# Kernel tuning notes

Hardware: AMD Instinct MI355X
Metric: run time of the kernel (lower is better)

The kernel has to match this reference:

```python
import jax, jax.numpy as jnp
import numpy as np
import math

GROUPS = 32
EPS = 1e-5

def group_norm(x, w, b):
    B, C, H, W = x.shape
    xg = x.reshape(B, GROUPS, C // GROUPS, H, W)
    mu = xg.mean(axis=(2, 3, 4), keepdims=True)
    var = xg.var(axis=(2, 3, 4), keepdims=True)
    xn = ((xg - mu) * jax.lax.rsqrt(var + EPS)).reshape(B, C, H, W)
    return xn * w[None, :, None, None] + b[None, :, None, None]

def conv1x1(x, w, b):
    # x: [B,Cin,H,W], w: [Cout,Cin], b: [Cout]
    return jnp.einsum('bchw,oc->bohw', x, w) + b[None, :, None, None]

def setup_inputs() -> dict:
    key = jax.random.key(0)
    ks = jax.random.split(key, 8)
    B, C, E, H, W = 8, 256, 512, 64, 64
    x = jax.random.normal(ks[0], (B, C, H, W), dtype=jnp.float32)
    condA = jax.random.normal(ks[1], (B, E, H, W), dtype=jnp.float32)
    gn_x_w = jnp.ones((C,), jnp.float32)
    gn_x_b = jnp.zeros((C,), jnp.float32)
    gn_c_w = jnp.ones((E,), jnp.float32)
    gn_c_b = jnp.zeros((E,), jnp.float32)
    q_w = jax.random.normal(ks[2], (C, C), jnp.float32) * 0.02
    q_b = jnp.zeros((C,), jnp.float32)
    k_w = jax.random.normal(ks[3], (C, E), jnp.float32) * 0.02
    k_b = jnp.zeros((C,), jnp.float32)
    v_w = jax.random.normal(ks[4], (C, E), jnp.float32) * 0.02
    v_b = jnp.zeros((C,), jnp.float32)
    return {"x": x, "condA": condA, "gn_x_w": gn_x_w, "gn_x_b": gn_x_b,
            "gn_c_w": gn_c_w, "gn_c_b": gn_c_b, "q_w": q_w, "q_b": q_b,
            "k_w": k_w, "k_b": k_b, "v_w": v_w, "v_b": v_b}

def reference(x, condA, gn_x_w, gn_x_b, gn_c_w, gn_c_b, q_w, q_b, k_w, k_b, v_w, v_b):
    B, C, H, W = x.shape
    scale = math.sqrt(C)
    h = group_norm(x, gn_x_w, gn_x_b)
    h1 = group_norm(condA, gn_c_w, gn_c_b)
    q = conv1x1(h, q_w, q_b)      # [B,C,H,W]
    k = conv1x1(h1, k_w, k_b)     # [B,C,Hc,Wc]
    v = conv1x1(h1, v_w, v_b)     # [B,C,Hc,Wc]
    qf = q.transpose(0, 2, 3, 1).reshape(B, H * W, C)        # [B,N,C]
    kf = k.reshape(B, C, -1)                                  # [B,C,M]
    vf = v.transpose(0, 2, 3, 1).reshape(B, -1, C)            # [B,M,C]
    attn = jax.nn.softmax(jnp.einsum('bnc,bcm->bnm', qf, kf) / scale, axis=-1)
    out = jnp.einsum('bnm,bmc->bnc', attn, vf)                # [B,N,C]
    return out.reshape(B, H, W, C).transpose(0, 3, 1, 2)
```

## Files before the change

kernel.cpp:

```cpp
#include <hip/hip_runtime.h>


typedef _Float16 half8 __attribute__((ext_vector_type(8)));
typedef _Float16 half4v __attribute__((ext_vector_type(4)));
typedef _Float16 half2v __attribute__((ext_vector_type(2)));
typedef float f32x4 __attribute__((ext_vector_type(4)));
typedef float f32x16 __attribute__((ext_vector_type(16)));
typedef unsigned u32x4v __attribute__((ext_vector_type(4)));

#define MFMA16(a, b, c) __builtin_amdgcn_mfma_f32_16x16x32_f16((a), (b), (c), 0, 0, 0)
#define MFMA32(a, b, c) __builtin_amdgcn_mfma_f32_32x32x16_f16((a), (b), (c), 0, 0, 0)

#define GLOAD_LDS(src, dst)                                                   \
  __builtin_amdgcn_global_load_lds(                                           \
      (const __attribute__((address_space(1))) unsigned*)(src),               \
      (__attribute__((address_space(3))) unsigned*)(dst), 16, 0, 0)

__global__ __launch_bounds__(256) void statswconv_kernel(
    const float* __restrict__ x, const float* __restrict__ condA,
    float* __restrict__ sx, float* __restrict__ sc,
    const float* __restrict__ wq, const float* __restrict__ wk,
    const float* __restrict__ wv, _Float16* __restrict__ wqt,
    _Float16* __restrict__ wkt, _Float16* __restrict__ wvt) {
  int bid = blockIdx.x;
  int t = threadIdx.x;
  if (bid >= 512) {
    int i = (bid - 512) * 256 + t;
    const float* src;
    _Float16* dst;
    int cin, ksbits, gi;
    if (i < 8192) { src = wq; dst = wqt; cin = 256; ksbits = 3; gi = i; }
    else if (i < 24576) { src = wk; dst = wkt; cin = 512; ksbits = 4; gi = i - 8192; }
    else { src = wv; dst = wvt; cin = 512; ksbits = 4; gi = i - 24576; }
    int tile = gi >> 6, g = gi & 63;
    int otile = tile >> ksbits, ks = tile & ((1 << ksbits) - 1);
    int o = otile * 16 + (g & 15), k = ks * 32 + (g >> 4) * 8;
    const float* s = src + (size_t)o * cin + k;
    half8 hv;
#pragma unroll
    for (int j = 0; j < 8; j++) hv[j] = (_Float16)s[j];
    *(half8*)(dst + (size_t)gi * 8) = hv;
    return;
  }
  const float4* src;
  int nf4;
  float* dst;
  float inv_n;
  if (bid < 256) {
    src = (const float4*)(x + (size_t)bid * 32768);
    nf4 = 8192;
    dst = sx + bid * 2;
    inv_n = 1.0f / 32768.0f;
  } else {
    int j = bid - 256;
    src = (const float4*)(condA + (size_t)j * 65536);
    nf4 = 16384;
    dst = sc + j * 2;
    inv_n = 1.0f / 65536.0f;
  }
  float s = 0.f, s2 = 0.f;
  for (int i = t; i < nf4; i += 256) {
    float4 v = src[i];
    s += v.x + v.y + v.z + v.w;
    s2 += v.x * v.x + v.y * v.y + v.z * v.z + v.w * v.w;
  }
#pragma unroll
  for (int m = 1; m <= 32; m <<= 1) {
    s += __shfl_xor(s, m, 64);
    s2 += __shfl_xor(s2, m, 64);
  }
  __shared__ float red[8];
  int w = t >> 6;
  if ((t & 63) == 0) { red[w * 2] = s; red[w * 2 + 1] = s2; }
  __syncthreads();
  if (t == 0) {
    float S = red[0] + red[2] + red[4] + red[6];
    float S2 = red[1] + red[3] + red[5] + red[7];
    float mu = S * inv_n;
    float var = S2 * inv_n - mu * mu;
    dst[0] = mu;
    dst[1] = rsqrtf(var + 1e-5f);
  }
}

__global__ __launch_bounds__(256) void ntrans_kernel(
    const float* __restrict__ x, const float* __restrict__ condA,
    const float* __restrict__ statsx, const float* __restrict__ statsc,
    const float* __restrict__ gxw, const float* __restrict__ gxb,
    const float* __restrict__ gcw, const float* __restrict__ gcb,
    _Float16* __restrict__ hxTt, _Float16* __restrict__ h1Tt) {
  int bid = blockIdx.x;
  const float *src, *stats, *gw, *gb;
  _Float16* dst;
  int CH, gsh, bid2;
  if (bid < 2048) {
    src = x; stats = statsx; gw = gxw; gb = gxb; dst = hxTt;
    CH = 256; gsh = 3; bid2 = bid;
  } else {
    src = condA; stats = statsc; gw = gcw; gb = gcb; dst = h1Tt;
    CH = 512; gsh = 4; bid2 = bid - 2048;
  }
  int b = bid2 & 7, nt = (bid2 >> 3) & 63, ctile = bid2 >> 9;
  int n0 = nt * 64, c0 = ctile * 64;
  int t = threadIdx.x;
  __shared__ float tile[64][65];

  int cl = t >> 2;
  int c = c0 + cl;
  const float* st = stats + ((size_t)b * 32 + (c >> gsh)) * 2;
  float mu = st[0], rs = st[1];
  float a = rs * gw[c];
  float bb = gb[c] - mu * a;
  const float* srow = src + ((size_t)(b * CH + c)) * 4096 + n0 + (t & 3) * 16;
#pragma unroll
  for (int i = 0; i < 4; i++) {
    float4 v = *(const float4*)(srow + 4 * i);
    int nn = (t & 3) * 16 + 4 * i;
    tile[cl][nn + 0] = v.x * a + bb;
    tile[cl][nn + 1] = v.y * a + bb;
    tile[cl][nn + 2] = v.z * a + bb;
    tile[cl][nn + 3] = v.w * a + bb;
  }
  __syncthreads();
  int nl = t >> 2;
  half8 ov[2];
#pragma unroll
  for (int u = 0; u < 2; u++)
#pragma unroll
    for (int i = 0; i < 8; i++) ov[u][i] = (_Float16)tile[(t & 3) * 16 + 8 * u + i][nl];
  int n = n0 + nl;
  size_t tb = ((size_t)b * 256 + (n >> 4)) * (CH >> 5);
  int ca = c0 + (t & 3) * 16;
#pragma unroll
  for (int u = 0; u < 2; u++) {
    int cc = ca + 8 * u;
    size_t addr = ((tb + (cc >> 5)) * 64 + (n & 15) + 16 * ((cc >> 3) & 3)) * 8;
    *(half8*)(dst + addr) = ov[u];
  }
}

__global__ __launch_bounds__(256, 2) void projQ_kernel(
    const _Float16* __restrict__ Ht, const _Float16* __restrict__ Wt,
    const float* __restrict__ bias, _Float16* __restrict__ Qt) {
  int bid = blockIdx.x;
  int b = bid & 7, nt = bid >> 3;
  int t = threadIdx.x, l = t & 63, w = t >> 6;
  int c15 = l & 15, q = l >> 4;

  __shared__ __align__(16) _Float16 hbuf[16384];
  half8* hb = (half8*)hbuf;
  {
    const half8* sg = (const half8*)Ht + (size_t)(b * 256 + nt * 4) * 512;
#pragma unroll
    for (int i = 0; i < 8; i++) hb[t + 256 * i] = sg[t + 256 * i];
  }
  __syncthreads();

  const half8* wt8 = (const half8*)Wt;
#pragma unroll
  for (int p = 0; p < 2; p++) {
    int oa = (p * 4 + w) * 2;
    f32x4 acc[2][4] = {};
#pragma unroll
    for (int ks = 0; ks < 8; ks++) {
      half8 af0 = wt8[((size_t)(oa + 0) * 8 + ks) * 64 + l];
      half8 af1 = wt8[((size_t)(oa + 1) * 8 + ks) * 64 + l];
#pragma unroll
      for (int nt2 = 0; nt2 < 4; nt2++) {
        half8 bf = hb[(nt2 * 8 + ks) * 64 + l];
        acc[0][nt2] = MFMA16(af0, bf, acc[0][nt2]);
        acc[1][nt2] = MFMA16(af1, bf, acc[1][nt2]);
      }
    }
#pragma unroll
    for (int j = 0; j < 2; j++) {
      int o4 = (oa + j) * 16 + 4 * q;
      f32x4 bv = *(const f32x4*)(bias + o4);
#pragma unroll
      for (int nt2 = 0; nt2 < 4; nt2++) {
        half4v hv;
#pragma unroll
        for (int r = 0; r < 4; r++) hv[r] = (_Float16)((acc[j][nt2][r] + bv[r]) * 0.0625f);
        size_t addr = ((((size_t)b * 128 + nt * 2 + (nt2 >> 1)) * 16 + (oa + j)) * 64 +
                       (nt2 & 1) * 16 + c15 + 32 * (q >> 1)) * 8 + (q & 1) * 4;
        *(half4v*)(Qt + addr) = hv;
      }
    }
  }
}

__global__ __launch_bounds__(256, 2) void projKV_kernel(
    const _Float16* __restrict__ Ht, const _Float16* __restrict__ Wk,
    const _Float16* __restrict__ Wv, const float* __restrict__ kb,
    const float* __restrict__ vb, _Float16* __restrict__ Kt,
    _Float16* __restrict__ Vt) {
  int bid = blockIdx.x;
  int b = bid & 7, mt = bid >> 3;
  int m0 = mt * 64;
  int t = threadIdx.x, l = t & 63, w = t >> 6;
  int c15 = l & 15, q = l >> 4;

  __shared__ __align__(16) _Float16 hbuf[32768];
  half8* hb = (half8*)hbuf;
  {
    const half8* sg = (const half8*)Ht + (size_t)(b * 256 + mt * 4) * 1024;
#pragma unroll
    for (int i = 0; i < 16; i++) hb[t + 256 * i] = sg[t + 256 * i];
  }
  __syncthreads();

  const half8* wk8 = (const half8*)Wk;
  const half8* wv8 = (const half8*)Wv;
#pragma unroll
  for (int p = 0; p < 2; p++) {
    int oa = (p * 4 + w) * 2;
    f32x4 acck[2][4] = {};
    f32x4 accv[4][2] = {};
#pragma unroll
    for (int ks = 0; ks < 16; ks++) {
      half8 kf0 = wk8[((size_t)(oa + 0) * 16 + ks) * 64 + l];
      half8 kf1 = wk8[((size_t)(oa + 1) * 16 + ks) * 64 + l];
      half8 vf0 = wv8[((size_t)(oa + 0) * 16 + ks) * 64 + l];
      half8 vf1 = wv8[((size_t)(oa + 1) * 16 + ks) * 64 + l];
#pragma unroll
      for (int nt2 = 0; nt2 < 4; nt2++) {
        half8 lf = hb[(nt2 * 16 + ks) * 64 + l];
        acck[0][nt2] = MFMA16(kf0, lf, acck[0][nt2]);
        acck[1][nt2] = MFMA16(kf1, lf, acck[1][nt2]);
        accv[nt2][0] = MFMA16(lf, vf0, accv[nt2][0]);
        accv[nt2][1] = MFMA16(lf, vf1, accv[nt2][1]);
      }
    }
#pragma unroll
    for (int j = 0; j < 2; j++) {
      int o4 = (oa + j) * 16 + 4 * q;
      f32x4 bv = *(const f32x4*)(kb + o4);
#pragma unroll
      for (int nt2 = 0; nt2 < 4; nt2++) {
        half4v hv;
#pragma unroll
        for (int r = 0; r < 4; r++) hv[r] = (_Float16)(acck[j][nt2][r] + bv[r]);
        size_t addr = ((((size_t)b * 128 + mt * 2 + (nt2 >> 1)) * 16 + (oa + j)) * 64 +
                       (nt2 & 1) * 16 + c15 + 32 * (q >> 1)) * 8 + (q & 1) * 4;
        *(half4v*)(Kt + addr) = hv;
      }
    }
#pragma unroll
    for (int nt2 = 0; nt2 < 4; nt2++) {
      int m = m0 + nt2 * 16 + 4 * q;
      size_t mbase = ((size_t)b * 256 + (m >> 4)) * 8;
#pragma unroll
      for (int j = 0; j < 2; j++) {
        int c = (oa + j) * 16 + c15;
        float bs = vb[c];
        half4v hv;
#pragma unroll
        for (int r = 0; r < 4; r++) hv[r] = (_Float16)(accv[nt2][j][r] + bs);
        size_t addr = ((mbase + (c >> 5)) * 64 + (c & 31) + ((q >> 1) << 5)) * 8 + (q & 1) * 4;
        *(half4v*)(Vt + addr) = hv;
      }
    }
  }
}

__global__ __launch_bounds__(256, 2) void attn_kernel(
    const _Float16* __restrict__ Qt, const _Float16* __restrict__ Kt,
    const _Float16* __restrict__ Vt, float* __restrict__ out,
    float* __restrict__ O1, float* __restrict__ l0g,
    float* __restrict__ l1g) {
  int bid = blockIdx.x;
  int b = bid & 7, nt = (bid >> 3) & 31, ms = bid >> 8;
  int n0 = nt * 128;
  int t = threadIdx.x, l = t & 63, nh = t >> 6;
  int l31 = l & 31, h = l >> 5;
  int it0 = ms * 64, it1 = it0 + 64;

  __shared__ __align__(16) _Float16 kbuf[2][8192];
  __shared__ __align__(16) _Float16 vbuf[2][8192];

  half8 qf[16];
  {
    const half8* qt8 =
        (const half8*)Qt + ((size_t)(b * 128 + nt * 4 + nh) * 16) * 64 + l;
#pragma unroll
    for (int ks = 0; ks < 16; ks++) qf[ks] = qt8[ks * 64];
  }

  const _Float16* ksrc = Kt + (size_t)b * 1048576;
  const _Float16* vsrc = Vt + (size_t)b * 1048576;

  f32x16 acc[8] = {};
  float l_part = 0.f;

#define STAGE(it)                                                          \
  {                                                                        \
    int bs_ = (it) & 1;                                                    \
    const _Float16* ks_ = ksrc + (size_t)(it) * 8192;                      \
    const _Float16* vs_ = vsrc + (size_t)(it) * 8192;                      \
    _Float16* kd_ = &kbuf[bs_][0];                                         \
    _Float16* vd_ = &vbuf[bs_][0];                                         \
    _Pragma("unroll") for (int r_ = 0; r_ < 4; r_++) {                     \
      GLOAD_LDS(ks_ + (t + 256 * r_) * 8, kd_ + (t + 256 * r_) * 8);       \
      GLOAD_LDS(vs_ + (t + 256 * r_) * 8, vd_ + (t + 256 * r_) * 8);       \
    }                                                                      \
  }

  STAGE(it0);
  __syncthreads();

  for (int it = it0; it < it1; it++) {
    int cur = it & 1;
    if (it + 1 < it1) STAGE(it + 1);

    const half8* kb = (const half8*)&kbuf[cur][0] + l;
    const half8* vb8 = (const half8*)&vbuf[cur][0] + l;

    f32x16 s = {};
#pragma unroll
    for (int g = 0; g < 4; g++) {
      half8 kf[4];
#pragma unroll
      for (int i = 0; i < 4; i++) kf[i] = kb[(g * 4 + i) * 64];
      __builtin_amdgcn_s_setprio(1);
#pragma unroll
      for (int i = 0; i < 4; i++) s = MFMA32(kf[i], qf[g * 4 + i], s);
      __builtin_amdgcn_s_setprio(0);
    }

    unsigned uo[8];
#pragma unroll
    for (int k2 = 0; k2 < 8; k2++) {
      float e0 = __expf(s[2 * k2]);
      float e1 = __expf(s[2 * k2 + 1]);
      l_part += e0 + e1;
      half2v h2 = {(_Float16)e0, (_Float16)e1};
      uo[k2] = __builtin_bit_cast(unsigned, h2);
    }
    unsigned x0 = uo[0], y0 = uo[2];
    asm("v_permlane32_swap_b32 %0, %1" : "+v"(x0), "+v"(y0));
    unsigned x1 = uo[1], y1 = uo[3];
    asm("v_permlane32_swap_b32 %0, %1" : "+v"(x1), "+v"(y1));
    unsigned x2 = uo[4], y2 = uo[6];
    asm("v_permlane32_swap_b32 %0, %1" : "+v"(x2), "+v"(y2));
    unsigned x3 = uo[5], y3 = uo[7];
    asm("v_permlane32_swap_b32 %0, %1" : "+v"(x3), "+v"(y3));
    u32x4v P0 = {x0, x1, y0, y1};
    u32x4v P1 = {x2, x3, y2, y3};
    half8 pf0 = __builtin_bit_cast(half8, P0);
    half8 pf1 = __builtin_bit_cast(half8, P1);

#pragma unroll
    for (int u = 0; u < 2; u++) {
      const half8* vv = vb8 + u * 512;
      half8 pfu = u ? pf1 : pf0;
#pragma unroll
      for (int g = 0; g < 2; g++) {
        half8 vf[4];
#pragma unroll
        for (int i = 0; i < 4; i++) vf[i] = vv[(g * 4 + i) * 64];
        __builtin_amdgcn_s_setprio(1);
#pragma unroll
        for (int i = 0; i < 4; i++)
          acc[g * 4 + i] = MFMA32(pfu, vf[i], acc[g * 4 + i]);
        __builtin_amdgcn_s_setprio(0);
      }
    }
    __syncthreads();
  }
#undef STAGE

  {
    float v = l_part + __shfl_xor(l_part, 32, 64);
    float* lG = ms ? l1g : l0g;
    if (l < 32) lG[b * 4096 + n0 + nh * 32 + l] = v;
  }
  float* ob = ms ? O1 : out;
#pragma unroll
  for (int cb = 0; cb < 8; cb++) {
    int c = cb * 32 + l31;
    float* orow = ob + ((size_t)(b * 256 + c)) * 4096 + n0 + nh * 32 + 4 * h;
#pragma unroll
    for (int k2 = 0; k2 < 4; k2++) {
      f32x4 o4;
#pragma unroll
      for (int r = 0; r < 4; r++) o4[r] = acc[cb][4 * k2 + r];
      *(f32x4*)(orow + 8 * k2) = o4;
    }
  }
}

__global__ __launch_bounds__(256) void combine_kernel(
    float* __restrict__ out, const float* __restrict__ O1,
    const float* __restrict__ l0g, const float* __restrict__ l1g) {
  size_t i = (size_t)blockIdx.x * 256 + threadIdx.x;
  f32x4 a = ((const f32x4*)out)[i];
  f32x4 b4 = ((const f32x4*)O1)[i];
  int bidx = (int)(i >> 18);
  int n4 = (int)(i & 1023);
  f32x4 La = ((const f32x4*)l0g)[bidx * 1024 + n4];
  f32x4 Lb = ((const f32x4*)l1g)[bidx * 1024 + n4];
  f32x4 r;
#pragma unroll
  for (int j = 0; j < 4; j++) r[j] = (a[j] + b4[j]) / (La[j] + Lb[j]);
  ((f32x4*)out)[i] = r;
}

extern "C" void kernel_launch(void* const* d_in, const int* in_sizes, int n_in,
                              void* d_out, int out_size, void* d_ws,
                              size_t ws_size, hipStream_t stream) {
  const float* x = (const float*)d_in[0];
  const float* condA = (const float*)d_in[1];
  const float* gxw = (const float*)d_in[2];
  const float* gxb = (const float*)d_in[3];
  const float* gcw = (const float*)d_in[4];
  const float* gcb = (const float*)d_in[5];
  const float* qw = (const float*)d_in[6];
  const float* qb = (const float*)d_in[7];
  const float* kw = (const float*)d_in[8];
  const float* kb = (const float*)d_in[9];
  const float* vw = (const float*)d_in[10];
  const float* vb = (const float*)d_in[11];
  float* out = (float*)d_out;

  char* ws = (char*)d_ws;
  float* statsx = (float*)(ws);
  float* statsc = (float*)(ws + 2048);
  _Float16* wqt = (_Float16*)(ws + 4096);
  _Float16* wkt = (_Float16*)(ws + 135168);
  _Float16* wvt = (_Float16*)(ws + 397312);
  char* p = ws + 659456;
  _Float16* hxTt = (_Float16*)p; p += (size_t)8 * 4096 * 256 * 2;
  _Float16* h1Tt = (_Float16*)p; p += (size_t)8 * 4096 * 512 * 2;
  _Float16* Qt = (_Float16*)p;   p += (size_t)8 * 4096 * 256 * 2;
  _Float16* Kt = (_Float16*)p;   p += (size_t)8 * 4096 * 256 * 2;
  _Float16* Vt = (_Float16*)p;

  float* O1 = (float*)(ws + 659456);
  float* l0g = (float*)(ws + 659456 + (size_t)33554432);
  float* l1g = (float*)(ws + 659456 + (size_t)33554432 + 131072);

  statswconv_kernel<<<672, 256, 0, stream>>>(x, condA, statsx, statsc,
                                             qw, kw, vw, wqt, wkt, wvt);
  ntrans_kernel<<<6144, 256, 0, stream>>>(x, condA, statsx, statsc,
                                          gxw, gxb, gcw, gcb, hxTt, h1Tt);
  projQ_kernel<<<512, 256, 0, stream>>>(hxTt, wqt, qb, Qt);
  projKV_kernel<<<512, 256, 0, stream>>>(h1Tt, wkt, wvt, kb, vb, Kt, Vt);
  attn_kernel<<<512, 256, 0, stream>>>(Qt, Kt, Vt, out, O1, l0g, l1g);
  combine_kernel<<<8192, 256, 0, stream>>>(out, O1, l0g, l1g);
}
```

Baseline: 383.2 us.

## Load V fragments directly from global into registers instead of LDS staging

The attention kernel stops staging V tiles through double-buffered shared memory. Each wave now reads its V MFMA operands straight from global memory into registers, issuing half before the QK^T step so the latency overlaps with compute. This halves LDS usage and removes the LDS write/read traffic for V. In exchange, every wave (4 per block) fetches the same V data redundantly from global/L2, register pressure rises with 16 extra half8 values, and the load latency may be exposed.

```diff
diff --git a/kernel.cpp b/kernel.cpp
--- a/kernel.cpp
+++ b/kernel.cpp
@@ -276,7 +276,6 @@
   int it0 = ms * 64, it1 = it0 + 64;
 
   __shared__ __align__(16) _Float16 kbuf[2][8192];
-  __shared__ __align__(16) _Float16 vbuf[2][8192];
 
   half8 qf[16];
   {
@@ -287,33 +286,34 @@
   }
 
   const _Float16* ksrc = Kt + (size_t)b * 1048576;
-  const _Float16* vsrc = Vt + (size_t)b * 1048576;
+  const half8* vg = (const half8*)(Vt + (size_t)b * 1048576) + l;
 
   f32x16 acc[8] = {};
   float l_part = 0.f;
 
-#define STAGE(it)                                                          \
+#define STAGE_K(it)                                                        \
   {                                                                        \
     int bs_ = (it) & 1;                                                    \
     const _Float16* ks_ = ksrc + (size_t)(it) * 8192;                      \
-    const _Float16* vs_ = vsrc + (size_t)(it) * 8192;                      \
     _Float16* kd_ = &kbuf[bs_][0];                                         \
-    _Float16* vd_ = &vbuf[bs_][0];                                         \
     _Pragma("unroll") for (int r_ = 0; r_ < 4; r_++) {                     \
       GLOAD_LDS(ks_ + (t + 256 * r_) * 8, kd_ + (t + 256 * r_) * 8);       \
-      GLOAD_LDS(vs_ + (t + 256 * r_) * 8, vd_ + (t + 256 * r_) * 8);       \
     }                                                                      \
   }
 
-  STAGE(it0);
+  STAGE_K(it0);
   __syncthreads();
 
   for (int it = it0; it < it1; it++) {
     int cur = it & 1;
-    if (it + 1 < it1) STAGE(it + 1);
+    if (it + 1 < it1) STAGE_K(it + 1);
 
     const half8* kb = (const half8*)&kbuf[cur][0] + l;
-    const half8* vb8 = (const half8*)&vbuf[cur][0] + l;
+    const half8* vt = vg + (size_t)it * 1024;
+
+    half8 vfA[8];
+#pragma unroll
+    for (int i = 0; i < 8; i++) vfA[i] = vt[i * 64];
 
     f32x16 s = {};
 #pragma unroll
@@ -349,25 +349,20 @@
     half8 pf0 = __builtin_bit_cast(half8, P0);
     half8 pf1 = __builtin_bit_cast(half8, P1);
 
-#pragma unroll
-    for (int u = 0; u < 2; u++) {
-      const half8* vv = vb8 + u * 512;
-      half8 pfu = u ? pf1 : pf0;
-#pragma unroll
-      for (int g = 0; g < 2; g++) {
-        half8 vf[4];
-#pragma unroll
-        for (int i = 0; i < 4; i++) vf[i] = vv[(g * 4 + i) * 64];
-        __builtin_amdgcn_s_setprio(1);
-#pragma unroll
-        for (int i = 0; i < 4; i++)
-          acc[g * 4 + i] = MFMA32(pfu, vf[i], acc[g * 4 + i]);
-        __builtin_amdgcn_s_setprio(0);
-      }
-    }
+    half8 vfB[8];
+#pragma unroll
+    for (int i = 0; i < 8; i++) vfB[i] = vt[(8 + i) * 64];
+    __builtin_amdgcn_s_setprio(1);
+#pragma unroll
+    for (int cb = 0; cb < 8; cb++) acc[cb] = MFMA32(pf0, vfA[cb], acc[cb]);
+    __builtin_amdgcn_s_setprio(0);
+    __builtin_amdgcn_s_setprio(1);
+#pragma unroll
+    for (int cb = 0; cb < 8; cb++) acc[cb] = MFMA32(pf1, vfB[cb], acc[cb]);
+    __builtin_amdgcn_s_setprio(0);
     __syncthreads();
   }
-#undef STAGE
+#undef STAGE_K
 
   {
     float v = l_part + __shfl_xor(l_part, 32, 64);
```

Result: slower. 459.3 us (+19.9%).

## Fuse group-norm apply and transpose into Q/KV projection kernels

Applied to the files above, without the earlier changes.

Removes the separate normalize-and-transpose kernel and the fp16 intermediate buffers it wrote. Each projection block now loads its fp32 input tile directly, applies group-norm scale/shift, and transposes through LDS into the MFMA fragment layout before the GEMM. This eliminates a global write and re-read of the normalized activations and one kernel launch, at the cost of extra LDS usage and a serialized load/transpose prologue with fewer blocks issuing the loads. The workspace layout is reorganized since the intermediates are gone.

```diff
diff --git a/kernel.cpp b/kernel.cpp
--- a/kernel.cpp
+++ b/kernel.cpp
@@ -83,79 +83,58 @@
   }
 }
 
-__global__ __launch_bounds__(256) void ntrans_kernel(
-    const float* __restrict__ x, const float* __restrict__ condA,
-    const float* __restrict__ statsx, const float* __restrict__ statsc,
-    const float* __restrict__ gxw, const float* __restrict__ gxb,
-    const float* __restrict__ gcw, const float* __restrict__ gcb,
-    _Float16* __restrict__ hxTt, _Float16* __restrict__ h1Tt) {
-  int bid = blockIdx.x;
-  const float *src, *stats, *gw, *gb;
-  _Float16* dst;
-  int CH, gsh, bid2;
-  if (bid < 2048) {
-    src = x; stats = statsx; gw = gxw; gb = gxb; dst = hxTt;
-    CH = 256; gsh = 3; bid2 = bid;
-  } else {
-    src = condA; stats = statsc; gw = gcw; gb = gcb; dst = h1Tt;
-    CH = 512; gsh = 4; bid2 = bid - 2048;
-  }
-  int b = bid2 & 7, nt = (bid2 >> 3) & 63, ctile = bid2 >> 9;
-  int n0 = nt * 64, c0 = ctile * 64;
-  int t = threadIdx.x;
-  __shared__ float tile[64][65];
-
-  int cl = t >> 2;
-  int c = c0 + cl;
-  const float* st = stats + ((size_t)b * 32 + (c >> gsh)) * 2;
-  float mu = st[0], rs = st[1];
-  float a = rs * gw[c];
-  float bb = gb[c] - mu * a;
-  const float* srow = src + ((size_t)(b * CH + c)) * 4096 + n0 + (t & 3) * 16;
-#pragma unroll
-  for (int i = 0; i < 4; i++) {
-    float4 v = *(const float4*)(srow + 4 * i);
-    int nn = (t & 3) * 16 + 4 * i;
-    tile[cl][nn + 0] = v.x * a + bb;
-    tile[cl][nn + 1] = v.y * a + bb;
-    tile[cl][nn + 2] = v.z * a + bb;
-    tile[cl][nn + 3] = v.w * a + bb;
-  }
-  __syncthreads();
-  int nl = t >> 2;
-  half8 ov[2];
-#pragma unroll
-  for (int u = 0; u < 2; u++)
-#pragma unroll
-    for (int i = 0; i < 8; i++) ov[u][i] = (_Float16)tile[(t & 3) * 16 + 8 * u + i][nl];
-  int n = n0 + nl;
-  size_t tb = ((size_t)b * 256 + (n >> 4)) * (CH >> 5);
-  int ca = c0 + (t & 3) * 16;
-#pragma unroll
-  for (int u = 0; u < 2; u++) {
-    int cc = ca + 8 * u;
-    size_t addr = ((tb + (cc >> 5)) * 64 + (n & 15) + 16 * ((cc >> 3) & 3)) * 8;
-    *(half8*)(dst + addr) = ov[u];
-  }
-}
-
 __global__ __launch_bounds__(256, 2) void projQ_kernel(
-    const _Float16* __restrict__ Ht, const _Float16* __restrict__ Wt,
-    const float* __restrict__ bias, _Float16* __restrict__ Qt) {
+    const float* __restrict__ x, const float* __restrict__ stats,
+    const float* __restrict__ gw, const float* __restrict__ gb,
+    const _Float16* __restrict__ Wt, const float* __restrict__ bias,
+    _Float16* __restrict__ Qt) {
   int bid = blockIdx.x;
   int b = bid & 7, nt = bid >> 3;
+  int n0 = nt * 64;
   int t = threadIdx.x, l = t & 63, w = t >> 6;
   int c15 = l & 15, q = l >> 4;
 
   __shared__ __align__(16) _Float16 hbuf[16384];
+  __shared__ _Float16 tile[64][65];
+
+  int cl = t >> 2;
+  int nl = t >> 2;
+  int nn0 = (t & 3) * 16;
+#pragma unroll
+  for (int ct = 0; ct < 4; ct++) {
+    int c0 = ct * 64;
+    int c = c0 + cl;
+    const float* st = stats + ((size_t)b * 32 + (c >> 3)) * 2;
+    float mu = st[0], rs = st[1];
+    float a = rs * gw[c];
+    float bb = gb[c] - mu * a;
+    const float* srow = x + ((size_t)(b * 256 + c)) * 4096 + n0 + nn0;
+#pragma unroll
+    for (int i = 0; i < 4; i++) {
+      float4 v = *(const float4*)(srow + 4 * i);
+      int nn = nn0 + 4 * i;
+      tile[cl][nn + 0] = (_Float16)(v.x * a + bb);
+      tile[cl][nn + 1] = (_Float16)(v.y * a + bb);
+      tile[cl][nn + 2] = (_Float16)(v.z * a + bb);
+      tile[cl][nn + 3] = (_Float16)(v.w * a + bb);
+    }
+    __syncthreads();
+    int nt2 = nl >> 4, g3 = nl & 15;
+#pragma unroll
+    for (int u = 0; u < 2; u++) {
+      int cl8 = nn0 + 8 * u;
+      int c8 = c0 + cl8;
+      int ks = c8 >> 5;
+      int g = g3 + 16 * ((c8 >> 3) & 3);
+      half8 ov;
+#pragma unroll
+      for (int i = 0; i < 8; i++) ov[i] = tile[cl8 + i][nl];
+      *(half8*)&hbuf[(((size_t)nt2 * 8 + ks) * 64 + g) * 8] = ov;
+    }
+    __syncthreads();
+  }
+
   half8* hb = (half8*)hbuf;
-  {
-    const half8* sg = (const half8*)Ht + (size_t)(b * 256 + nt * 4) * 512;
-#pragma unroll
-    for (int i = 0; i < 8; i++) hb[t + 256 * i] = sg[t + 256 * i];
-  }
-  __syncthreads();
-
   const half8* wt8 = (const half8*)Wt;
 #pragma unroll
   for (int p = 0; p < 2; p++) {
@@ -190,10 +169,11 @@
 }
 
 __global__ __launch_bounds__(256, 2) void projKV_kernel(
-    const _Float16* __restrict__ Ht, const _Float16* __restrict__ Wk,
-    const _Float16* __restrict__ Wv, const float* __restrict__ kb,
-    const float* __restrict__ vb, _Float16* __restrict__ Kt,
-    _Float16* __restrict__ Vt) {
+    const float* __restrict__ condA, const float* __restrict__ stats,
+    const float* __restrict__ gw, const float* __restrict__ gb,
+    const _Float16* __restrict__ Wk, const _Float16* __restrict__ Wv,
+    const float* __restrict__ kb, const float* __restrict__ vb,
+    _Float16* __restrict__ Kt, _Float16* __restrict__ Vt) {
   int bid = blockIdx.x;
   int b = bid & 7, mt = bid >> 3;
   int m0 = mt * 64;
@@ -201,14 +181,46 @@
   int c15 = l & 15, q = l >> 4;
 
   __shared__ __align__(16) _Float16 hbuf[32768];
+  __shared__ _Float16 tile[64][65];
+
+  int cl = t >> 2;
+  int nl = t >> 2;
+  int nn0 = (t & 3) * 16;
+#pragma unroll
+  for (int ct = 0; ct < 8; ct++) {
+    int c0 = ct * 64;
+    int c = c0 + cl;
+    const float* st = stats + ((size_t)b * 32 + (c >> 4)) * 2;
+    float mu = st[0], rs = st[1];
+    float a = rs * gw[c];
+    float bb = gb[c] - mu * a;
+    const float* srow = condA + ((size_t)(b * 512 + c)) * 4096 + m0 + nn0;
+#pragma unroll
+    for (int i = 0; i < 4; i++) {
+      float4 v = *(const float4*)(srow + 4 * i);
+      int nn = nn0 + 4 * i;
+      tile[cl][nn + 0] = (_Float16)(v.x * a + bb);
+      tile[cl][nn + 1] = (_Float16)(v.y * a + bb);
+      tile[cl][nn + 2] = (_Float16)(v.z * a + bb);
+      tile[cl][nn + 3] = (_Float16)(v.w * a + bb);
+    }
+    __syncthreads();
+    int nt2 = nl >> 4, g3 = nl & 15;
+#pragma unroll
+    for (int u = 0; u < 2; u++) {
+      int cl8 = nn0 + 8 * u;
+      int c8 = c0 + cl8;
+      int ks = c8 >> 5;
+      int g = g3 + 16 * ((c8 >> 3) & 3);
+      half8 ov;
+#pragma unroll
+      for (int i = 0; i < 8; i++) ov[i] = tile[cl8 + i][nl];
+      *(half8*)&hbuf[(((size_t)nt2 * 16 + ks) * 64 + g) * 8] = ov;
+    }
+    __syncthreads();
+  }
+
   half8* hb = (half8*)hbuf;
-  {
-    const half8* sg = (const half8*)Ht + (size_t)(b * 256 + mt * 4) * 1024;
-#pragma unroll
-    for (int i = 0; i < 16; i++) hb[t + 256 * i] = sg[t + 256 * i];
-  }
-  __syncthreads();
-
   const half8* wk8 = (const half8*)Wk;
   const half8* wv8 = (const half8*)Wv;
 #pragma unroll
@@ -429,22 +441,18 @@
   _Float16* wkt = (_Float16*)(ws + 135168);
   _Float16* wvt = (_Float16*)(ws + 397312);
   char* p = ws + 659456;
-  _Float16* hxTt = (_Float16*)p; p += (size_t)8 * 4096 * 256 * 2;
-  _Float16* h1Tt = (_Float16*)p; p += (size_t)8 * 4096 * 512 * 2;
-  _Float16* Qt = (_Float16*)p;   p += (size_t)8 * 4096 * 256 * 2;
-  _Float16* Kt = (_Float16*)p;   p += (size_t)8 * 4096 * 256 * 2;
-  _Float16* Vt = (_Float16*)p;
-
-  float* O1 = (float*)(ws + 659456);
-  float* l0g = (float*)(ws + 659456 + (size_t)33554432);
-  float* l1g = (float*)(ws + 659456 + (size_t)33554432 + 131072);
+  float* O1 = (float*)p;
+  float* l0g = (float*)(p + (size_t)33554432);
+  float* l1g = (float*)(p + (size_t)33554432 + 131072);
+  _Float16* Qt = (_Float16*)(p + (size_t)33554432 + 262144);
+  _Float16* Kt = (_Float16*)(p + (size_t)33554432 + 262144 + 16777216);
+  _Float16* Vt = (_Float16*)(p + (size_t)33554432 + 262144 + 2 * 16777216);
 
   statswconv_kernel<<<672, 256, 0, stream>>>(x, condA, statsx, statsc,
                                              qw, kw, vw, wqt, wkt, wvt);
-  ntrans_kernel<<<6144, 256, 0, stream>>>(x, condA, statsx, statsc,
-                                          gxw, gxb, gcw, gcb, hxTt, h1Tt);
-  projQ_kernel<<<512, 256, 0, stream>>>(hxTt, wqt, qb, Qt);
-  projKV_kernel<<<512, 256, 0, stream>>>(h1Tt, wkt, wvt, kb, vb, Kt, Vt);
+  projQ_kernel<<<512, 256, 0, stream>>>(x, statsx, gxw, gxb, wqt, qb, Qt);
+  projKV_kernel<<<512, 256, 0, stream>>>(condA, statsc, gcw, gcb, wkt, wvt,
+                                         kb, vb, Kt, Vt);
   attn_kernel<<<512, 256, 0, stream>>>(Qt, Kt, Vt, out, O1, l0g, l1g);
   combine_kernel<<<8192, 256, 0, stream>>>(out, O1, l0g, l1g);
 }
```

After: 370.8 us. -3.2%, faster.
